# Kernel optimization log

Measured on AMD Instinct MI355X. Metric: run time of the kernel, lower is better.

## Reference

```python
import jax, jax.numpy as jnp
import numpy as np

N_NODES = 50000
NEG_SLOPE = 0.2


def _gat_conv(x, src, dst, W, a_src, a_dst, b, num_nodes):
    # W: [H*C, F_in]; a_src/a_dst: [H, C]; b: [H*C]
    H, C = a_src.shape
    xp = (x @ W.T).reshape(num_nodes, H, C)              # [N,H,C]
    alpha_s = jnp.sum(xp * a_src[None], axis=-1)          # [N,H]
    alpha_d = jnp.sum(xp * a_dst[None], axis=-1)          # [N,H]
    e = jax.nn.leaky_relu(alpha_s[src] + alpha_d[dst], NEG_SLOPE)  # [E,H]
    # segment softmax over incoming edges of each dst node (self-loops guarantee non-empty segments)
    m = jax.ops.segment_max(e, dst, num_segments=num_nodes)
    e = jnp.exp(e - m[dst])
    s = jax.ops.segment_sum(e, dst, num_segments=num_nodes)
    alpha = e / s[dst]                                    # [E,H]
    out = jax.ops.segment_sum(alpha[:, :, None] * xp[src], dst, num_segments=num_nodes)  # [N,H,C]
    return out.reshape(num_nodes, H * C) + b


def setup_inputs() -> dict:
    key = jax.random.key(0)
    ks = jax.random.split(key, 12)
    N, E, F_in, HID, H, Z = N_NODES, 800000, 128, 64, 2, 32
    sc = 0.1
    return {
        "features": jax.random.normal(ks[0], (N, F_in), jnp.float32),
        "edges": jax.random.randint(ks[1], (2, E), 0, N, jnp.int32),
        "W1": jax.random.normal(ks[2], (H * HID, F_in), jnp.float32) * sc,
        "a_src1": jax.random.normal(ks[3], (H, HID), jnp.float32) * sc,
        "a_dst1": jax.random.normal(ks[4], (H, HID), jnp.float32) * sc,
        "b1": jnp.zeros((H * HID,), jnp.float32),
        "W_mu": jax.random.normal(ks[5], (Z, H * HID), jnp.float32) * sc,
        "a_src_mu": jax.random.normal(ks[6], (1, Z), jnp.float32) * sc,
        "a_dst_mu": jax.random.normal(ks[7], (1, Z), jnp.float32) * sc,
        "b_mu": jnp.zeros((Z,), jnp.float32),
        "W_std": jax.random.normal(ks[8], (Z, H * HID), jnp.float32) * sc,
        "a_src_std": jax.random.normal(ks[9], (1, Z), jnp.float32) * sc,
        "a_dst_std": jax.random.normal(ks[10], (1, Z), jnp.float32) * sc,
        "b_std": jnp.zeros((Z,), jnp.float32),
    }


def reference(features, edges, W1, a_src1, a_dst1, b1, W_mu, a_src_mu, a_dst_mu, b_mu, W_std, a_src_std, a_dst_std, b_std):
    N = features.shape[0]
    loops = jnp.arange(N, dtype=edges.dtype)
    src = jnp.concatenate([edges[0], loops])  # add self loops (PyG default)
    dst = jnp.concatenate([edges[1], loops])
    h = _gat_conv(features, src, dst, W1, a_src1, a_dst1, b1, N)
    h = jax.nn.relu(h)  # dropout p=0.0 -> identity
    mu = _gat_conv(h, src, dst, W_mu, a_src_mu, a_dst_mu, b_mu, N)
    std = _gat_conv(h, src, dst, W_std, a_src_std, a_dst_std, b_std, N)
    return (mu, std)
```

## Files before the change

kernel.cpp:

```cpp
#include <hip/hip_runtime.h>
#include <math.h>

#define N_NODES 50000
#define N_EDGES 800000
#define ET (N_EDGES + N_NODES)
#define KD 128
#define Z 32
#define SH 7
#define BW 128
#define NBUCK ((N_NODES + BW - 1) / BW)
#define CHUNK 4096
#define NBLKA ((ET + CHUNK - 1) / CHUNK)
#define MTOT (NBUCK * NBLKA)
#define MBS ((MTOT + 1023) / 1024)

typedef __attribute__((ext_vector_type(8))) short bf16x8;
typedef __attribute__((ext_vector_type(4))) float f32x4;

static __device__ __forceinline__ float lrelu(float x){ return x > 0.f ? x : 0.2f*x; }
static __device__ __forceinline__ float lof(unsigned int u){ return __uint_as_float(u << 16); }
static __device__ __forceinline__ float hif(unsigned int u){ return __uint_as_float(u & 0xffff0000u); }
static __device__ __forceinline__ unsigned short f2bf(float f){
  unsigned int x = __float_as_uint(f);
  return (unsigned short)((x + 0x7fffu + ((x >> 16) & 1u)) >> 16);
}
static __device__ __forceinline__ unsigned int pack2(float lo, float hi){
  return (unsigned int)f2bf(lo) | ((unsigned int)f2bf(hi) << 16);
}

__global__ __launch_bounds__(256) void bhistA_kernel(const int* __restrict__ edges, int* __restrict__ M){
  int k = blockIdx.x, t = threadIdx.x;
  __shared__ int cnt[NBUCK];
  for(int b = t; b < NBUCK; b += 256) cnt[b] = 0;
  __syncthreads();
  int base = k*CHUNK;
  int lim = min(base + CHUNK, ET);
  for(int i = base + t; i < lim; i += 256){
    int d = (i < N_EDGES) ? edges[N_EDGES + i] : (i - N_EDGES);
    atomicAdd(&cnt[d >> SH], 1);
  }
  __syncthreads();
  for(int b = t; b < NBUCK; b += 256) M[b*NBLKA + k] = cnt[b];
}

__global__ __launch_bounds__(256) void scanM1_kernel(const int* __restrict__ M, int* __restrict__ bsumM){
  int b = blockIdx.x, t = threadIdx.x;
  int base = b*1024 + t*4;
  int s = 0;
  #pragma unroll
  for(int i=0;i<4;i++){ int n = base+i; if(n < MTOT) s += M[n]; }
  for(int off=32; off; off>>=1) s += __shfl_xor(s, off);
  __shared__ int ws[4];
  if((t&63)==0) ws[t>>6] = s;
  __syncthreads();
  if(t==0) bsumM[b] = ws[0]+ws[1]+ws[2]+ws[3];
}

__global__ __launch_bounds__(256) void scanM2_kernel(const int* __restrict__ bsumM, int* __restrict__ bpreM){
  __shared__ int sm[256];
  int t = threadIdx.x;
  int v = (t < MBS) ? bsumM[t] : 0;
  sm[t] = v;
  __syncthreads();
  for(int off=1; off<256; off<<=1){
    int u = (t >= off) ? sm[t-off] : 0;
    __syncthreads();
    sm[t] += u;
    __syncthreads();
  }
  if(t < MBS) bpreM[t] = sm[t] - v;
}

__global__ __launch_bounds__(256) void scanM3_kernel(const int* __restrict__ M, const int* __restrict__ bpreM,
                                                     int* __restrict__ Mpos){
  int b = blockIdx.x, t = threadIdx.x;
  int lane = t & 63, wv = t >> 6;
  int base = b*1024 + t*4;
  int d[4]; int s = 0;
  #pragma unroll
  for(int i=0;i<4;i++){ int n = base+i; d[i] = (n < MTOT) ? M[n] : 0; s += d[i]; }
  int v = s;
  for(int off=1; off<64; off<<=1){
    int u = __shfl_up(v, off);
    if(lane >= off) v += u;
  }
  int texcl = v - s;
  __shared__ int wtot[4];
  if(lane == 63) wtot[wv] = v;
  __syncthreads();
  int woff = 0;
  for(int i=0;i<wv;i++) woff += wtot[i];
  int run = bpreM[b] + woff + texcl;
  #pragma unroll
  for(int i=0;i<4;i++){
    int n = base+i;
    if(n < MTOT){ Mpos[n] = run; run += d[i]; }
  }
}

__global__ __launch_bounds__(256) void bplaceA_kernel(const int* __restrict__ edges, const int* __restrict__ Mpos,
                                                      int2* __restrict__ etmp){
  int k = blockIdx.x, t = threadIdx.x;
  __shared__ int cur[NBUCK];
  for(int b = t; b < NBUCK; b += 256) cur[b] = Mpos[b*NBLKA + k];
  __syncthreads();
  int base = k*CHUNK;
  int lim = min(base + CHUNK, ET);
  for(int i = base + t; i < lim; i += 256){
    int s, d;
    if(i < N_EDGES){ s = edges[i]; d = edges[N_EDGES+i]; } else { s = d = i - N_EDGES; }
    int pos = atomicAdd(&cur[d >> SH], 1);
    etmp[pos] = make_int2(s, d);
  }
}

__global__ __launch_bounds__(256) void bfin_kernel(const int* __restrict__ Mpos, const int2* __restrict__ etmp,
                                                   int* __restrict__ rowptr, int* __restrict__ esrc,
                                                   int* __restrict__ edst){
  int b = blockIdx.x, t = threadIdx.x;
  __shared__ int cnt[BW];
  __shared__ int pre[BW];
  __shared__ int lcur[BW];
  if(t < BW) cnt[t] = 0;
  if(b == 0 && t < 32) esrc[ET + t] = 0;
  __syncthreads();
  int beg = Mpos[b*NBLKA];
  int end = (b+1 < NBUCK) ? Mpos[(b+1)*NBLKA] : ET;
  for(int i = beg + t; i < end; i += 256) atomicAdd(&cnt[etmp[i].y & (BW-1)], 1);
  __syncthreads();
  if(t < BW) pre[t] = cnt[t];
  __syncthreads();
  for(int off=1; off<BW; off<<=1){
    int u = 0;
    if(t < BW && t >= off) u = pre[t-off];
    __syncthreads();
    if(t < BW) pre[t] += u;
    __syncthreads();
  }
  if(t < BW){
    int excl = pre[t] - cnt[t];
    int node = b*BW + t;
    if(node < N_NODES) rowptr[node] = beg + excl;
    lcur[t] = beg + excl;
  }
  if(b == 0 && t == 255) rowptr[N_NODES] = ET;
  __syncthreads();
  for(int i = beg + t; i < end; i += 256){
    int2 e = etmp[i];
    int pos = atomicAdd(&lcur[e.y & (BW-1)], 1);
    esrc[pos] = e.x;
    edst[pos] = e.y;
  }
}

__global__ __launch_bounds__(256) void wconv_kernel(const float* __restrict__ W1,
                                                    const float* __restrict__ Wmu, const float* __restrict__ Wst,
                                                    unsigned short* __restrict__ Wb1, unsigned short* __restrict__ Wb2){
  int i = blockIdx.x*256 + threadIdx.x;
  if(i < 128*KD) Wb1[i] = f2bf(W1[i]);
  if(i < 64*KD) Wb2[i] = f2bf(i < 32*KD ? Wmu[i] : Wst[i - 32*KD]);
}

__global__ __launch_bounds__(256) void mmt1_kernel(const float* __restrict__ X,
                                                   const unsigned short* __restrict__ Wb,
                                                   const float* __restrict__ asv, const float* __restrict__ adv,
                                                   unsigned short* __restrict__ outb,
                                                   float* __restrict__ as1, float* __restrict__ ad1){
  constexpr int OC = 128, CT = 8;
  int t = threadIdx.x;
  int w = t >> 6, L = t & 63;
  int col = L & 15, quad = L >> 4;
  int row0 = blockIdx.x*64 + w*16;
  int rA = row0 + col;
  if(rA >= N_NODES) rA = N_NODES-1;

  f32x4 acc[CT];
  #pragma unroll
  for(int ct=0;ct<CT;ct++) acc[ct] = (f32x4){0.f,0.f,0.f,0.f};

  #pragma unroll
  for(int kc=0;kc<4;kc++){
    int k0 = kc*32 + quad*8;
    const float* Xf = X + (size_t)rA*KD + k0;
    float4 p = *(const float4*)Xf;
    float4 q = *(const float4*)(Xf + 4);
    bf16x8 a;
    a[0] = (short)f2bf(p.x); a[1] = (short)f2bf(p.y);
    a[2] = (short)f2bf(p.z); a[3] = (short)f2bf(p.w);
    a[4] = (short)f2bf(q.x); a[5] = (short)f2bf(q.y);
    a[6] = (short)f2bf(q.z); a[7] = (short)f2bf(q.w);
    #pragma unroll
    for(int ct=0;ct<CT;ct++){
      bf16x8 b = *(const bf16x8*)(Wb + (size_t)(ct*16 + col)*KD + k0);
      acc[ct] = __builtin_amdgcn_mfma_f32_16x16x32_bf16(a, b, acc[ct], 0, 0, 0);
    }
  }

  float av[CT], dv[CT];
  #pragma unroll
  for(int ct=0;ct<CT;ct++){ av[ct] = asv[ct*16 + col]; dv[ct] = adv[ct*16 + col]; }

  #pragma unroll
  for(int r=0;r<4;r++){
    int row = row0 + quad*4 + r;
    #pragma unroll
    for(int ct=0;ct<CT;ct++)
      if(row < N_NODES) outb[(size_t)row*OC + ct*16 + col] = f2bf(acc[ct][r]);
    float s0 = acc[0][r]*av[0] + acc[1][r]*av[1] + acc[2][r]*av[2] + acc[3][r]*av[3];
    float s1 = acc[4][r]*av[4] + acc[5][r]*av[5] + acc[6][r]*av[6] + acc[7][r]*av[7];
    float d0 = acc[0][r]*dv[0] + acc[1][r]*dv[1] + acc[2][r]*dv[2] + acc[3][r]*dv[3];
    float d1 = acc[4][r]*dv[4] + acc[5][r]*dv[5] + acc[6][r]*dv[6] + acc[7][r]*dv[7];
    #pragma unroll
    for(int off=1; off<16; off<<=1){
      s0 += __shfl_xor(s0, off); s1 += __shfl_xor(s1, off);
      d0 += __shfl_xor(d0, off); d1 += __shfl_xor(d1, off);
    }
    if(col == 0 && row < N_NODES){
      as1[row*2] = s0; as1[row*2+1] = s1;
      ad1[row*2] = d0; ad1[row*2+1] = d1;
    }
  }
}

__global__ __launch_bounds__(256) void mmt2_kernel(const unsigned short* __restrict__ Xb,
                                                   const unsigned short* __restrict__ Wb,
                                                   const float* __restrict__ asmu, const float* __restrict__ admu,
                                                   const float* __restrict__ asst, const float* __restrict__ adst,
                                                   unsigned short* __restrict__ outb,
                                                   float* __restrict__ as2, float* __restrict__ ad2){
  constexpr int OC = 64, CT = 4;
  int t = threadIdx.x;
  int w = t >> 6, L = t & 63;
  int col = L & 15, quad = L >> 4;
  int row0 = blockIdx.x*64 + w*16;
  int rA = row0 + col;
  if(rA >= N_NODES) rA = N_NODES-1;

  f32x4 acc[CT];
  #pragma unroll
  for(int ct=0;ct<CT;ct++) acc[ct] = (f32x4){0.f,0.f,0.f,0.f};

  #pragma unroll
  for(int kc=0;kc<4;kc++){
    int k0 = kc*32 + quad*8;
    bf16x8 a = *(const bf16x8*)(Xb + (size_t)rA*KD + k0);
    #pragma unroll
    for(int ct=0;ct<CT;ct++){
      bf16x8 b = *(const bf16x8*)(Wb + (size_t)(ct*16 + col)*KD + k0);
      acc[ct] = __builtin_amdgcn_mfma_f32_16x16x32_bf16(a, b, acc[ct], 0, 0, 0);
    }
  }

  float av[CT], dv[CT];
  #pragma unroll
  for(int ct=0;ct<CT;ct++){
    av[ct] = (ct < 2) ? asmu[ct*16 + col] : asst[(ct-2)*16 + col];
    dv[ct] = (ct < 2) ? admu[ct*16 + col] : adst[(ct-2)*16 + col];
  }

  #pragma unroll
  for(int r=0;r<4;r++){
    int row = row0 + quad*4 + r;
    #pragma unroll
    for(int ct=0;ct<CT;ct++)
      if(row < N_NODES) outb[(size_t)row*OC + ct*16 + col] = f2bf(acc[ct][r]);
    float smu = acc[0][r]*av[0] + acc[1][r]*av[1];
    float sst = acc[2][r]*av[2] + acc[3][r]*av[3];
    float dmu = acc[0][r]*dv[0] + acc[1][r]*dv[1];
    float dst = acc[2][r]*dv[2] + acc[3][r]*dv[3];
    #pragma unroll
    for(int off=1; off<16; off<<=1){
      smu += __shfl_xor(smu, off); sst += __shfl_xor(sst, off);
      dmu += __shfl_xor(dmu, off); dst += __shfl_xor(dst, off);
    }
    if(col == 0 && row < N_NODES){
      as2[row*2] = smu; as2[row*2+1] = sst;
      ad2[row*2] = dmu; ad2[row*2+1] = dst;
    }
  }
}

__global__ __launch_bounds__(256) void wcalc_kernel(const int* __restrict__ esrc, const int* __restrict__ edst,
                                                    const float* __restrict__ as, const float* __restrict__ ad,
                                                    float2* __restrict__ wp){
  int i = blockIdx.x*256 + threadIdx.x;
  if(i >= ET) return;
  int s = esrc[i], d = edst[i];
  float2 a = ((const float2*)as)[s];
  float2 b = ((const float2*)ad)[d];
  wp[i] = make_float2(__expf(lrelu(a.x + b.x)), __expf(lrelu(a.y + b.y)));
}

__global__ __launch_bounds__(256) void agg1_kernel(const int* __restrict__ rowptr, const int* __restrict__ esrc,
                                                   const float2* __restrict__ wp,
                                                   const uint4* __restrict__ xb4,
                                                   const float* __restrict__ b1, uint4* __restrict__ hb4){
  int node = blockIdx.x*4 + (threadIdx.x>>6);
  int l = threadIdx.x & 63;
  if(node >= N_NODES) return;
  int g = l >> 4, c = l & 15;
  int beg = rowptr[node], end = rowptr[node+1];
  int n = end - beg;
  float a0=0.f,a1=0.f,a2=0.f,a3=0.f,a4=0.f,a5=0.f,a6=0.f,a7=0.f;
  float s0=0.f, s1=0.f;

#define S1_STEP(IDX) { \
    int e_ = esrc[(IDX)]; \
    float2 w_ = wp[(IDX)]; \
    uint4 u_ = xb4[(size_t)e_*16 + c]; \
    s0 += w_.x; s1 += w_.y; \
    float vv = (c < 8) ? w_.x : w_.y; \
    a0 += vv*lof(u_.x); a1 += vv*hif(u_.x); \
    a2 += vv*lof(u_.y); a3 += vv*hif(u_.y); \
    a4 += vv*lof(u_.z); a5 += vv*hif(u_.z); \
    a6 += vv*lof(u_.w); a7 += vv*hif(u_.w); }

#define S1_STEPM(IDX) { \
    int e_ = esrc[(IDX)]; \
    float2 w_ = wp[(IDX)]; \
    uint4 u_ = xb4[(size_t)e_*16 + c]; \
    float wx_ = ((IDX) < end) ? w_.x : 0.f; \
    float wy_ = ((IDX) < end) ? w_.y : 0.f; \
    s0 += wx_; s1 += wy_; \
    float vv = (c < 8) ? wx_ : wy_; \
    a0 += vv*lof(u_.x); a1 += vv*hif(u_.x); \
    a2 += vv*lof(u_.y); a3 += vv*hif(u_.y); \
    a4 += vv*lof(u_.z); a5 += vv*hif(u_.z); \
    a6 += vv*lof(u_.w); a7 += vv*hif(u_.w); }

  int i = beg;
  int nfull = n & ~7;
  for(; i < beg + nfull; i += 8){
    S1_STEP(i + g)
    S1_STEP(i + 4 + g)
  }
  if(i < end){
    S1_STEPM(i + g)
    S1_STEPM(i + 4 + g)
  }
#undef S1_STEP
#undef S1_STEPM

  #pragma unroll
  for(int off=16; off<64; off<<=1){
    s0 += __shfl_xor(s0,off); s1 += __shfl_xor(s1,off);
    a0 += __shfl_xor(a0,off); a1 += __shfl_xor(a1,off);
    a2 += __shfl_xor(a2,off); a3 += __shfl_xor(a3,off);
    a4 += __shfl_xor(a4,off); a5 += __shfl_xor(a5,off);
    a6 += __shfl_xor(a6,off); a7 += __shfl_xor(a7,off);
  }
  if(g == 0){
    float sd = (c < 8) ? s0 : s1;
    float inv = 1.f / sd;
    const float4* bp = (const float4*)(b1 + 8*c);
    float4 bl = bp[0], bh = bp[1];
    float r0 = fmaxf(a0*inv + bl.x, 0.f);
    float r1 = fmaxf(a1*inv + bl.y, 0.f);
    float r2 = fmaxf(a2*inv + bl.z, 0.f);
    float r3 = fmaxf(a3*inv + bl.w, 0.f);
    float r4 = fmaxf(a4*inv + bh.x, 0.f);
    float r5 = fmaxf(a5*inv + bh.y, 0.f);
    float r6 = fmaxf(a6*inv + bh.z, 0.f);
    float r7 = fmaxf(a7*inv + bh.w, 0.f);
    uint4 o;
    o.x = pack2(r0, r1); o.y = pack2(r2, r3);
    o.z = pack2(r4, r5); o.w = pack2(r6, r7);
    hb4[(size_t)node*16 + c] = o;
  }
}

__global__ __launch_bounds__(256) void agg2_kernel(const int* __restrict__ rowptr, const int* __restrict__ esrc,
                                                   const float2* __restrict__ wp,
                                                   const uint4* __restrict__ xb4,
                                                   const float* __restrict__ bmu, const float* __restrict__ bst,
                                                   float* __restrict__ out){
  int node = blockIdx.x*4 + (threadIdx.x>>6);
  int l = threadIdx.x & 63;
  if(node >= N_NODES) return;
  int g = l >> 3, c = l & 7;
  int beg = rowptr[node], end = rowptr[node+1];
  int n = end - beg;
  float a0=0.f,a1=0.f,a2=0.f,a3=0.f,a4=0.f,a5=0.f,a6=0.f,a7=0.f;
  float smu=0.f, sst=0.f;

#define S2_STEP(IDX) { \
    int e_ = esrc[(IDX)]; \
    float2 w_ = wp[(IDX)]; \
    uint4 u_ = xb4[(size_t)e_*8 + c]; \
    smu += w_.x; sst += w_.y; \
    float vv = (c < 4) ? w_.x : w_.y; \
    a0 += vv*lof(u_.x); a1 += vv*hif(u_.x); \
    a2 += vv*lof(u_.y); a3 += vv*hif(u_.y); \
    a4 += vv*lof(u_.z); a5 += vv*hif(u_.z); \
    a6 += vv*lof(u_.w); a7 += vv*hif(u_.w); }

#define S2_STEPM(IDX) { \
    int e_ = esrc[(IDX)]; \
    float2 w_ = wp[(IDX)]; \
    uint4 u_ = xb4[(size_t)e_*8 + c]; \
    float wx_ = ((IDX) < end) ? w_.x : 0.f; \
    float wy_ = ((IDX) < end) ? w_.y : 0.f; \
    smu += wx_; sst += wy_; \
    float vv = (c < 4) ? wx_ : wy_; \
    a0 += vv*lof(u_.x); a1 += vv*hif(u_.x); \
    a2 += vv*lof(u_.y); a3 += vv*hif(u_.y); \
    a4 += vv*lof(u_.z); a5 += vv*hif(u_.z); \
    a6 += vv*lof(u_.w); a7 += vv*hif(u_.w); }

  int i = beg;
  int nfull = n & ~15;
  for(; i < beg + nfull; i += 16){
    S2_STEP(i + g)
    S2_STEP(i + 8 + g)
  }
  if(i < end){
    S2_STEPM(i + g)
    S2_STEPM(i + 8 + g)
  }
#undef S2_STEP
#undef S2_STEPM

  #pragma unroll
  for(int off=8; off<64; off<<=1){
    smu += __shfl_xor(smu,off); sst += __shfl_xor(sst,off);
    a0 += __shfl_xor(a0,off); a1 += __shfl_xor(a1,off);
    a2 += __shfl_xor(a2,off); a3 += __shfl_xor(a3,off);
    a4 += __shfl_xor(a4,off); a5 += __shfl_xor(a5,off);
    a6 += __shfl_xor(a6,off); a7 += __shfl_xor(a7,off);
  }
  if(g == 0){
    float sd = (c < 4) ? smu : sst;
    float inv = 1.f / sd;
    const float* bb = (c < 4) ? (bmu + 8*c) : (bst + 8*(c-4));
    float4 bl = *(const float4*)bb;
    float4 bh = *(const float4*)(bb + 4);
    float* op = (c < 4) ? (out + (size_t)node*Z + 8*c)
                        : (out + (size_t)N_NODES*Z + (size_t)node*Z + 8*(c-4));
    float4 r0, r1;
    r0.x = a0*inv + bl.x; r0.y = a1*inv + bl.y;
    r0.z = a2*inv + bl.z; r0.w = a3*inv + bl.w;
    r1.x = a4*inv + bh.x; r1.y = a5*inv + bh.y;
    r1.z = a6*inv + bh.z; r1.w = a7*inv + bh.w;
    *(float4*)op = r0;
    *((float4*)op + 1) = r1;
  }
}

extern "C" void kernel_launch(void* const* d_in, const int* in_sizes, int n_in,
                              void* d_out, int out_size, void* d_ws, size_t ws_size,
                              hipStream_t stream){
  const float* x    = (const float*)d_in[0];
  const int*   edges= (const int*)d_in[1];
  const float* W1   = (const float*)d_in[2];
  const float* as1v = (const float*)d_in[3];
  const float* ad1v = (const float*)d_in[4];
  const float* b1   = (const float*)d_in[5];
  const float* Wmu  = (const float*)d_in[6];
  const float* asmu = (const float*)d_in[7];
  const float* admu = (const float*)d_in[8];
  const float* bmu  = (const float*)d_in[9];
  const float* Wst  = (const float*)d_in[10];
  const float* asst = (const float*)d_in[11];
  const float* adst = (const float*)d_in[12];
  const float* bst  = (const float*)d_in[13];
  float* out = (float*)d_out;

  char* p = (char*)d_ws;
  auto alloc = [&](size_t bytes)->char*{ char* r = p; p += (bytes + 255) & ~size_t(255); return r; };
  int*   M      = (int*)  alloc((size_t)MTOT*4);
  int*   Mpos   = (int*)  alloc((size_t)MTOT*4);
  int*   bsumM  = (int*)  alloc((size_t)MBS*4);
  int*   bpreM  = (int*)  alloc((size_t)MBS*4);
  int2*  etmp   = (int2*) alloc((size_t)(ET+32)*8);
  int*   esrc   = (int*)  alloc((size_t)(ET+32)*4);
  int*   edst   = (int*)  alloc((size_t)ET*4);
  int*   rowptr = (int*)  alloc((size_t)(N_NODES+1)*4);
  unsigned short* Wb1 = (unsigned short*)alloc((size_t)128*KD*2);
  unsigned short* Wb2 = (unsigned short*)alloc((size_t)64*KD*2);
  unsigned short* xpb1 = (unsigned short*)alloc((size_t)N_NODES*128*2);
  float* as1    = (float*)alloc((size_t)N_NODES*2*4);
  float* ad1    = (float*)alloc((size_t)N_NODES*2*4);
  unsigned short* hb = (unsigned short*)alloc((size_t)N_NODES*128*2);
  float* as2    = (float*)alloc((size_t)N_NODES*2*4);
  float* ad2    = (float*)alloc((size_t)N_NODES*2*4);
  unsigned short* xpb2 = xpb1;
  float2* wedge = (float2*)etmp;

  bhistA_kernel  <<<NBLKA, 256, 0, stream>>>(edges, M);
  scanM1_kernel  <<<MBS, 256, 0, stream>>>(M, bsumM);
  scanM2_kernel  <<<1, 256, 0, stream>>>(bsumM, bpreM);
  scanM3_kernel  <<<MBS, 256, 0, stream>>>(M, bpreM, Mpos);
  bplaceA_kernel <<<NBLKA, 256, 0, stream>>>(edges, Mpos, etmp);
  bfin_kernel    <<<NBUCK, 256, 0, stream>>>(Mpos, etmp, rowptr, esrc, edst);

  wconv_kernel   <<<(128*KD + 255)/256, 256, 0, stream>>>(W1, Wmu, Wst, Wb1, Wb2);

  mmt1_kernel  <<<(N_NODES+63)/64, 256, 0, stream>>>(x, Wb1, as1v, ad1v, xpb1, as1, ad1);
  wcalc_kernel <<<(ET+255)/256, 256, 0, stream>>>(esrc, edst, as1, ad1, wedge);
  agg1_kernel  <<<(N_NODES+3)/4, 256, 0, stream>>>(rowptr, esrc, wedge, (const uint4*)xpb1, b1, (uint4*)hb);

  mmt2_kernel  <<<(N_NODES+63)/64, 256, 0, stream>>>(hb, Wb2, asmu, admu, asst, adst, xpb1, as2, ad2);
  wcalc_kernel <<<(ET+255)/256, 256, 0, stream>>>(esrc, edst, as2, ad2, wedge);
  agg2_kernel  <<<(N_NODES+3)/4, 256, 0, stream>>>(rowptr, esrc, wedge, (const uint4*)xpb2, bmu, bst, out);
}
```

Measured before the change: 238.8 us.

## Replace two-level bucket sort CSR build with global atomic histogram and scatter

The CSR construction changes from a six-kernel two-level bucketed counting sort to a simpler pipeline: a global per-node atomic degree histogram, a single-block 1024-thread scan, and a scatter that uses global atomics on per-node cursors. Degree zeroing and padding init are folded into the weight-conversion kernel, so there are fewer launches and no intermediate etmp pass. In exchange it relies on global atomics with possible contention, a serial single-block scan, and nondeterministic edge order within each row, which can change floating-point summation order. The edge-weight buffer gets its own allocation instead of aliasing etmp.

```diff
diff --git a/kernel.cpp b/kernel.cpp
--- a/kernel.cpp
+++ b/kernel.cpp
@@ -6,13 +6,6 @@
 #define ET (N_EDGES + N_NODES)
 #define KD 128
 #define Z 32
-#define SH 7
-#define BW 128
-#define NBUCK ((N_NODES + BW - 1) / BW)
-#define CHUNK 4096
-#define NBLKA ((ET + CHUNK - 1) / CHUNK)
-#define MTOT (NBUCK * NBLKA)
-#define MBS ((MTOT + 1023) / 1024)
 
 typedef __attribute__((ext_vector_type(8))) short bf16x8;
 typedef __attribute__((ext_vector_type(4))) float f32x4;
@@ -28,137 +21,67 @@
   return (unsigned int)f2bf(lo) | ((unsigned int)f2bf(hi) << 16);
 }
 
-__global__ __launch_bounds__(256) void bhistA_kernel(const int* __restrict__ edges, int* __restrict__ M){
-  int k = blockIdx.x, t = threadIdx.x;
-  __shared__ int cnt[NBUCK];
-  for(int b = t; b < NBUCK; b += 256) cnt[b] = 0;
-  __syncthreads();
-  int base = k*CHUNK;
-  int lim = min(base + CHUNK, ET);
-  for(int i = base + t; i < lim; i += 256){
-    int d = (i < N_EDGES) ? edges[N_EDGES + i] : (i - N_EDGES);
-    atomicAdd(&cnt[d >> SH], 1);
-  }
-  __syncthreads();
-  for(int b = t; b < NBUCK; b += 256) M[b*NBLKA + k] = cnt[b];
-}
-
-__global__ __launch_bounds__(256) void scanM1_kernel(const int* __restrict__ M, int* __restrict__ bsumM){
-  int b = blockIdx.x, t = threadIdx.x;
-  int base = b*1024 + t*4;
+__global__ __launch_bounds__(256) void wconv_kernel(const float* __restrict__ W1,
+                                                    const float* __restrict__ Wmu, const float* __restrict__ Wst,
+                                                    unsigned short* __restrict__ Wb1, unsigned short* __restrict__ Wb2,
+                                                    int* __restrict__ deg, int* __restrict__ esrc){
+  int i = blockIdx.x*256 + threadIdx.x;
+  if(i < 128*KD) Wb1[i] = f2bf(W1[i]);
+  if(i < 64*KD) Wb2[i] = f2bf(i < 32*KD ? Wmu[i] : Wst[i - 32*KD]);
+  if(i < N_NODES) deg[i] = 0;
+  if(i < 32) esrc[ET + i] = 0;
+}
+
+__global__ __launch_bounds__(256) void ghist_kernel(const int* __restrict__ edges, int* __restrict__ deg){
+  int i = blockIdx.x*256 + threadIdx.x;
+  if(i >= ET) return;
+  int d = (i < N_EDGES) ? edges[N_EDGES + i] : (i - N_EDGES);
+  atomicAdd(&deg[d], 1);
+}
+
+__global__ __launch_bounds__(1024) void gscan_kernel(const int* __restrict__ deg,
+                                                     int* __restrict__ rowptr, int* __restrict__ cur){
+  constexpr int CHK = (N_NODES + 1023) / 1024;
+  int t = threadIdx.x;
+  int lane = t & 63, wv = t >> 6;
+  int base = t * CHK;
+  int d[CHK];
   int s = 0;
   #pragma unroll
-  for(int i=0;i<4;i++){ int n = base+i; if(n < MTOT) s += M[n]; }
-  for(int off=32; off; off>>=1) s += __shfl_xor(s, off);
-  __shared__ int ws[4];
-  if((t&63)==0) ws[t>>6] = s;
-  __syncthreads();
-  if(t==0) bsumM[b] = ws[0]+ws[1]+ws[2]+ws[3];
-}
-
-__global__ __launch_bounds__(256) void scanM2_kernel(const int* __restrict__ bsumM, int* __restrict__ bpreM){
-  __shared__ int sm[256];
-  int t = threadIdx.x;
-  int v = (t < MBS) ? bsumM[t] : 0;
-  sm[t] = v;
-  __syncthreads();
-  for(int off=1; off<256; off<<=1){
-    int u = (t >= off) ? sm[t-off] : 0;
-    __syncthreads();
-    sm[t] += u;
-    __syncthreads();
-  }
-  if(t < MBS) bpreM[t] = sm[t] - v;
-}
-
-__global__ __launch_bounds__(256) void scanM3_kernel(const int* __restrict__ M, const int* __restrict__ bpreM,
-                                                     int* __restrict__ Mpos){
-  int b = blockIdx.x, t = threadIdx.x;
-  int lane = t & 63, wv = t >> 6;
-  int base = b*1024 + t*4;
-  int d[4]; int s = 0;
-  #pragma unroll
-  for(int i=0;i<4;i++){ int n = base+i; d[i] = (n < MTOT) ? M[n] : 0; s += d[i]; }
+  for(int i=0;i<CHK;i++){
+    int n = base + i;
+    int v = (n < N_NODES) ? deg[n] : 0;
+    d[i] = v; s += v;
+  }
   int v = s;
   for(int off=1; off<64; off<<=1){
     int u = __shfl_up(v, off);
     if(lane >= off) v += u;
   }
-  int texcl = v - s;
-  __shared__ int wtot[4];
-  if(lane == 63) wtot[wv] = v;
+  __shared__ int wt[16];
+  if(lane == 63) wt[wv] = v;
   __syncthreads();
   int woff = 0;
-  for(int i=0;i<wv;i++) woff += wtot[i];
-  int run = bpreM[b] + woff + texcl;
-  #pragma unroll
-  for(int i=0;i<4;i++){
-    int n = base+i;
-    if(n < MTOT){ Mpos[n] = run; run += d[i]; }
-  }
-}
-
-__global__ __launch_bounds__(256) void bplaceA_kernel(const int* __restrict__ edges, const int* __restrict__ Mpos,
-                                                      int2* __restrict__ etmp){
-  int k = blockIdx.x, t = threadIdx.x;
-  __shared__ int cur[NBUCK];
-  for(int b = t; b < NBUCK; b += 256) cur[b] = Mpos[b*NBLKA + k];
-  __syncthreads();
-  int base = k*CHUNK;
-  int lim = min(base + CHUNK, ET);
-  for(int i = base + t; i < lim; i += 256){
-    int s, d;
-    if(i < N_EDGES){ s = edges[i]; d = edges[N_EDGES+i]; } else { s = d = i - N_EDGES; }
-    int pos = atomicAdd(&cur[d >> SH], 1);
-    etmp[pos] = make_int2(s, d);
-  }
-}
-
-__global__ __launch_bounds__(256) void bfin_kernel(const int* __restrict__ Mpos, const int2* __restrict__ etmp,
-                                                   int* __restrict__ rowptr, int* __restrict__ esrc,
-                                                   int* __restrict__ edst){
-  int b = blockIdx.x, t = threadIdx.x;
-  __shared__ int cnt[BW];
-  __shared__ int pre[BW];
-  __shared__ int lcur[BW];
-  if(t < BW) cnt[t] = 0;
-  if(b == 0 && t < 32) esrc[ET + t] = 0;
-  __syncthreads();
-  int beg = Mpos[b*NBLKA];
-  int end = (b+1 < NBUCK) ? Mpos[(b+1)*NBLKA] : ET;
-  for(int i = beg + t; i < end; i += 256) atomicAdd(&cnt[etmp[i].y & (BW-1)], 1);
-  __syncthreads();
-  if(t < BW) pre[t] = cnt[t];
-  __syncthreads();
-  for(int off=1; off<BW; off<<=1){
-    int u = 0;
-    if(t < BW && t >= off) u = pre[t-off];
-    __syncthreads();
-    if(t < BW) pre[t] += u;
-    __syncthreads();
-  }
-  if(t < BW){
-    int excl = pre[t] - cnt[t];
-    int node = b*BW + t;
-    if(node < N_NODES) rowptr[node] = beg + excl;
-    lcur[t] = beg + excl;
-  }
-  if(b == 0 && t == 255) rowptr[N_NODES] = ET;
-  __syncthreads();
-  for(int i = beg + t; i < end; i += 256){
-    int2 e = etmp[i];
-    int pos = atomicAdd(&lcur[e.y & (BW-1)], 1);
-    esrc[pos] = e.x;
-    edst[pos] = e.y;
-  }
-}
-
-__global__ __launch_bounds__(256) void wconv_kernel(const float* __restrict__ W1,
-                                                    const float* __restrict__ Wmu, const float* __restrict__ Wst,
-                                                    unsigned short* __restrict__ Wb1, unsigned short* __restrict__ Wb2){
+  for(int i=0;i<wv;i++) woff += wt[i];
+  int run = woff + (v - s);
+  #pragma unroll
+  for(int i=0;i<CHK;i++){
+    int n = base + i;
+    if(n < N_NODES){ rowptr[n] = run; cur[n] = run; }
+    run += d[i];
+  }
+  if(t == 1023) rowptr[N_NODES] = run;
+}
+
+__global__ __launch_bounds__(256) void gplace_kernel(const int* __restrict__ edges, int* __restrict__ cur,
+                                                     int* __restrict__ esrc, int* __restrict__ edst){
   int i = blockIdx.x*256 + threadIdx.x;
-  if(i < 128*KD) Wb1[i] = f2bf(W1[i]);
-  if(i < 64*KD) Wb2[i] = f2bf(i < 32*KD ? Wmu[i] : Wst[i - 32*KD]);
+  if(i >= ET) return;
+  int s, d;
+  if(i < N_EDGES){ s = edges[i]; d = edges[N_EDGES+i]; } else { s = d = i - N_EDGES; }
+  int pos = atomicAdd(&cur[d], 1);
+  esrc[pos] = s;
+  edst[pos] = d;
 }
 
 __global__ __launch_bounds__(256) void mmt1_kernel(const float* __restrict__ X,
@@ -467,14 +390,12 @@
 
   char* p = (char*)d_ws;
   auto alloc = [&](size_t bytes)->char*{ char* r = p; p += (bytes + 255) & ~size_t(255); return r; };
-  int*   M      = (int*)  alloc((size_t)MTOT*4);
-  int*   Mpos   = (int*)  alloc((size_t)MTOT*4);
-  int*   bsumM  = (int*)  alloc((size_t)MBS*4);
-  int*   bpreM  = (int*)  alloc((size_t)MBS*4);
-  int2*  etmp   = (int2*) alloc((size_t)(ET+32)*8);
+  int*   deg    = (int*)  alloc((size_t)N_NODES*4);
+  int*   cur    = (int*)  alloc((size_t)N_NODES*4);
+  int*   rowptr = (int*)  alloc((size_t)(N_NODES+1)*4);
   int*   esrc   = (int*)  alloc((size_t)(ET+32)*4);
   int*   edst   = (int*)  alloc((size_t)ET*4);
-  int*   rowptr = (int*)  alloc((size_t)(N_NODES+1)*4);
+  float2* wedge = (float2*)alloc((size_t)(ET+32)*8);
   unsigned short* Wb1 = (unsigned short*)alloc((size_t)128*KD*2);
   unsigned short* Wb2 = (unsigned short*)alloc((size_t)64*KD*2);
   unsigned short* xpb1 = (unsigned short*)alloc((size_t)N_NODES*128*2);
@@ -484,16 +405,11 @@
   float* as2    = (float*)alloc((size_t)N_NODES*2*4);
   float* ad2    = (float*)alloc((size_t)N_NODES*2*4);
   unsigned short* xpb2 = xpb1;
-  float2* wedge = (float2*)etmp;
-
-  bhistA_kernel  <<<NBLKA, 256, 0, stream>>>(edges, M);
-  scanM1_kernel  <<<MBS, 256, 0, stream>>>(M, bsumM);
-  scanM2_kernel  <<<1, 256, 0, stream>>>(bsumM, bpreM);
-  scanM3_kernel  <<<MBS, 256, 0, stream>>>(M, bpreM, Mpos);
-  bplaceA_kernel <<<NBLKA, 256, 0, stream>>>(edges, Mpos, etmp);
-  bfin_kernel    <<<NBUCK, 256, 0, stream>>>(Mpos, etmp, rowptr, esrc, edst);
-
-  wconv_kernel   <<<(128*KD + 255)/256, 256, 0, stream>>>(W1, Wmu, Wst, Wb1, Wb2);
+
+  wconv_kernel  <<<(N_NODES+255)/256, 256, 0, stream>>>(W1, Wmu, Wst, Wb1, Wb2, deg, esrc);
+  ghist_kernel  <<<(ET+255)/256, 256, 0, stream>>>(edges, deg);
+  gscan_kernel  <<<1, 1024, 0, stream>>>(deg, rowptr, cur);
+  gplace_kernel <<<(ET+255)/256, 256, 0, stream>>>(edges, cur, esrc, edst);
 
   mmt1_kernel  <<<(N_NODES+63)/64, 256, 0, stream>>>(x, Wb1, as1v, ad1v, xpb1, as1, ad1);
   wcalc_kernel <<<(ET+255)/256, 256, 0, stream>>>(esrc, edst, as1, ad1, wedge);
```

Measured after the change: 363.8 us. +52.3%, slower.

## Merge independent CSR-build and GEMM kernels into shared launches, pack edge temp

Applied to the files above, without the earlier changes.

Launches the bucket histogram together with the weight bf16 conversion in one grid, and the bucket placement together with the first-layer GEMM in another, with the block index picking the role. This removes two launches and lets independent work overlap. The temporary edge array shrinks from int2 to a packed 32-bit word (17-bit source, local destination in the high bits), which halves its traffic in placement and finalisation. The edge-weight buffer now gets its own allocation because it can no longer alias the smaller temp array. Packing assumes node ids fit in 17 bits.

```diff
diff --git a/kernel.cpp b/kernel.cpp
--- a/kernel.cpp
+++ b/kernel.cpp
@@ -13,6 +13,7 @@
 #define NBLKA ((ET + CHUNK - 1) / CHUNK)
 #define MTOT (NBUCK * NBLKA)
 #define MBS ((MTOT + 1023) / 1024)
+#define WCB 64
 
 typedef __attribute__((ext_vector_type(8))) short bf16x8;
 typedef __attribute__((ext_vector_type(4))) float f32x4;
@@ -28,8 +29,8 @@
   return (unsigned int)f2bf(lo) | ((unsigned int)f2bf(hi) << 16);
 }
 
-__global__ __launch_bounds__(256) void bhistA_kernel(const int* __restrict__ edges, int* __restrict__ M){
-  int k = blockIdx.x, t = threadIdx.x;
+static __device__ __forceinline__ void bhistA_body(int k, const int* __restrict__ edges, int* __restrict__ M){
+  int t = threadIdx.x;
   __shared__ int cnt[NBUCK];
   for(int b = t; b < NBUCK; b += 256) cnt[b] = 0;
   __syncthreads();
@@ -41,6 +42,22 @@
   }
   __syncthreads();
   for(int b = t; b < NBUCK; b += 256) M[b*NBLKA + k] = cnt[b];
+}
+
+static __device__ __forceinline__ void wconv_body(int bid, const float* __restrict__ W1,
+                                                  const float* __restrict__ Wmu, const float* __restrict__ Wst,
+                                                  unsigned short* __restrict__ Wb1, unsigned short* __restrict__ Wb2){
+  int i = bid*256 + threadIdx.x;
+  if(i < 128*KD) Wb1[i] = f2bf(W1[i]);
+  if(i < 64*KD) Wb2[i] = f2bf(i < 32*KD ? Wmu[i] : Wst[i - 32*KD]);
+}
+
+__global__ __launch_bounds__(256) void packA_kernel(const int* __restrict__ edges, int* __restrict__ M,
+                                                    const float* __restrict__ W1,
+                                                    const float* __restrict__ Wmu, const float* __restrict__ Wst,
+                                                    unsigned short* __restrict__ Wb1, unsigned short* __restrict__ Wb2){
+  if(blockIdx.x < NBLKA) bhistA_body(blockIdx.x, edges, M);
+  else                   wconv_body(blockIdx.x - NBLKA, W1, Wmu, Wst, Wb1, Wb2);
 }
 
 __global__ __launch_bounds__(256) void scanM1_kernel(const int* __restrict__ M, int* __restrict__ bsumM){
@@ -98,9 +115,9 @@
   }
 }
 
-__global__ __launch_bounds__(256) void bplaceA_kernel(const int* __restrict__ edges, const int* __restrict__ Mpos,
-                                                      int2* __restrict__ etmp){
-  int k = blockIdx.x, t = threadIdx.x;
+static __device__ __forceinline__ void bplaceA_body(int k, const int* __restrict__ edges,
+                                                    const int* __restrict__ Mpos, unsigned int* __restrict__ etmp){
+  int t = threadIdx.x;
   __shared__ int cur[NBUCK];
   for(int b = t; b < NBUCK; b += 256) cur[b] = Mpos[b*NBLKA + k];
   __syncthreads();
@@ -110,67 +127,20 @@
     int s, d;
     if(i < N_EDGES){ s = edges[i]; d = edges[N_EDGES+i]; } else { s = d = i - N_EDGES; }
     int pos = atomicAdd(&cur[d >> SH], 1);
-    etmp[pos] = make_int2(s, d);
-  }
-}
-
-__global__ __launch_bounds__(256) void bfin_kernel(const int* __restrict__ Mpos, const int2* __restrict__ etmp,
-                                                   int* __restrict__ rowptr, int* __restrict__ esrc,
-                                                   int* __restrict__ edst){
-  int b = blockIdx.x, t = threadIdx.x;
-  __shared__ int cnt[BW];
-  __shared__ int pre[BW];
-  __shared__ int lcur[BW];
-  if(t < BW) cnt[t] = 0;
-  if(b == 0 && t < 32) esrc[ET + t] = 0;
-  __syncthreads();
-  int beg = Mpos[b*NBLKA];
-  int end = (b+1 < NBUCK) ? Mpos[(b+1)*NBLKA] : ET;
-  for(int i = beg + t; i < end; i += 256) atomicAdd(&cnt[etmp[i].y & (BW-1)], 1);
-  __syncthreads();
-  if(t < BW) pre[t] = cnt[t];
-  __syncthreads();
-  for(int off=1; off<BW; off<<=1){
-    int u = 0;
-    if(t < BW && t >= off) u = pre[t-off];
-    __syncthreads();
-    if(t < BW) pre[t] += u;
-    __syncthreads();
-  }
-  if(t < BW){
-    int excl = pre[t] - cnt[t];
-    int node = b*BW + t;
-    if(node < N_NODES) rowptr[node] = beg + excl;
-    lcur[t] = beg + excl;
-  }
-  if(b == 0 && t == 255) rowptr[N_NODES] = ET;
-  __syncthreads();
-  for(int i = beg + t; i < end; i += 256){
-    int2 e = etmp[i];
-    int pos = atomicAdd(&lcur[e.y & (BW-1)], 1);
-    esrc[pos] = e.x;
-    edst[pos] = e.y;
-  }
-}
-
-__global__ __launch_bounds__(256) void wconv_kernel(const float* __restrict__ W1,
-                                                    const float* __restrict__ Wmu, const float* __restrict__ Wst,
-                                                    unsigned short* __restrict__ Wb1, unsigned short* __restrict__ Wb2){
-  int i = blockIdx.x*256 + threadIdx.x;
-  if(i < 128*KD) Wb1[i] = f2bf(W1[i]);
-  if(i < 64*KD) Wb2[i] = f2bf(i < 32*KD ? Wmu[i] : Wst[i - 32*KD]);
-}
-
-__global__ __launch_bounds__(256) void mmt1_kernel(const float* __restrict__ X,
-                                                   const unsigned short* __restrict__ Wb,
-                                                   const float* __restrict__ asv, const float* __restrict__ adv,
-                                                   unsigned short* __restrict__ outb,
-                                                   float* __restrict__ as1, float* __restrict__ ad1){
+    etmp[pos] = (unsigned int)s | ((unsigned int)(d & (BW-1)) << 17);
+  }
+}
+
+static __device__ __forceinline__ void mmt1_body(int bid, const float* __restrict__ X,
+                                                 const unsigned short* __restrict__ Wb,
+                                                 const float* __restrict__ asv, const float* __restrict__ adv,
+                                                 unsigned short* __restrict__ outb,
+                                                 float* __restrict__ as1, float* __restrict__ ad1){
   constexpr int OC = 128, CT = 8;
   int t = threadIdx.x;
   int w = t >> 6, L = t & 63;
   int col = L & 15, quad = L >> 4;
-  int row0 = blockIdx.x*64 + w*16;
+  int row0 = bid*64 + w*16;
   int rA = row0 + col;
   if(rA >= N_NODES) rA = N_NODES-1;
 
@@ -222,6 +192,56 @@
   }
 }
 
+__global__ __launch_bounds__(256) void packB_kernel(const int* __restrict__ edges, const int* __restrict__ Mpos,
+                                                    unsigned int* __restrict__ etmp,
+                                                    const float* __restrict__ X, const unsigned short* __restrict__ Wb,
+                                                    const float* __restrict__ asv, const float* __restrict__ adv,
+                                                    unsigned short* __restrict__ outb,
+                                                    float* __restrict__ as1, float* __restrict__ ad1){
+  if(blockIdx.x < NBLKA) bplaceA_body(blockIdx.x, edges, Mpos, etmp);
+  else                   mmt1_body(blockIdx.x - NBLKA, X, Wb, asv, adv, outb, as1, ad1);
+}
+
+__global__ __launch_bounds__(256) void bfin_kernel(const int* __restrict__ Mpos, const unsigned int* __restrict__ etmp,
+                                                   int* __restrict__ rowptr, int* __restrict__ esrc,
+                                                   int* __restrict__ edst){
+  int b = blockIdx.x, t = threadIdx.x;
+  __shared__ int cnt[BW];
+  __shared__ int pre[BW];
+  __shared__ int lcur[BW];
+  if(t < BW) cnt[t] = 0;
+  if(b == 0 && t < 32) esrc[ET + t] = 0;
+  __syncthreads();
+  int beg = Mpos[b*NBLKA];
+  int end = (b+1 < NBUCK) ? Mpos[(b+1)*NBLKA] : ET;
+  for(int i = beg + t; i < end; i += 256) atomicAdd(&cnt[etmp[i] >> 17], 1);
+  __syncthreads();
+  if(t < BW) pre[t] = cnt[t];
+  __syncthreads();
+  for(int off=1; off<BW; off<<=1){
+    int u = 0;
+    if(t < BW && t >= off) u = pre[t-off];
+    __syncthreads();
+    if(t < BW) pre[t] += u;
+    __syncthreads();
+  }
+  if(t < BW){
+    int excl = pre[t] - cnt[t];
+    int node = b*BW + t;
+    if(node < N_NODES) rowptr[node] = beg + excl;
+    lcur[t] = beg + excl;
+  }
+  if(b == 0 && t == 255) rowptr[N_NODES] = ET;
+  __syncthreads();
+  for(int i = beg + t; i < end; i += 256){
+    unsigned int e = etmp[i];
+    int lo = (int)(e >> 17);
+    int pos = atomicAdd(&lcur[lo], 1);
+    esrc[pos] = (int)(e & 0x1FFFFu);
+    edst[pos] = b*BW + lo;
+  }
+}
+
 __global__ __launch_bounds__(256) void mmt2_kernel(const unsigned short* __restrict__ Xb,
                                                    const unsigned short* __restrict__ Wb,
                                                    const float* __restrict__ asmu, const float* __restrict__ admu,
@@ -471,10 +491,11 @@
   int*   Mpos   = (int*)  alloc((size_t)MTOT*4);
   int*   bsumM  = (int*)  alloc((size_t)MBS*4);
   int*   bpreM  = (int*)  alloc((size_t)MBS*4);
-  int2*  etmp   = (int2*) alloc((size_t)(ET+32)*8);
+  unsigned int* etmp = (unsigned int*)alloc((size_t)ET*4);
   int*   esrc   = (int*)  alloc((size_t)(ET+32)*4);
   int*   edst   = (int*)  alloc((size_t)ET*4);
   int*   rowptr = (int*)  alloc((size_t)(N_NODES+1)*4);
+  float2* wedge = (float2*)alloc((size_t)(ET+32)*8);
   unsigned short* Wb1 = (unsigned short*)alloc((size_t)128*KD*2);
   unsigned short* Wb2 = (unsigned short*)alloc((size_t)64*KD*2);
   unsigned short* xpb1 = (unsigned short*)alloc((size_t)N_NODES*128*2);
@@ -484,18 +505,15 @@
   float* as2    = (float*)alloc((size_t)N_NODES*2*4);
   float* ad2    = (float*)alloc((size_t)N_NODES*2*4);
   unsigned short* xpb2 = xpb1;
-  float2* wedge = (float2*)etmp;
-
-  bhistA_kernel  <<<NBLKA, 256, 0, stream>>>(edges, M);
-  scanM1_kernel  <<<MBS, 256, 0, stream>>>(M, bsumM);
-  scanM2_kernel  <<<1, 256, 0, stream>>>(bsumM, bpreM);
-  scanM3_kernel  <<<MBS, 256, 0, stream>>>(M, bpreM, Mpos);
-  bplaceA_kernel <<<NBLKA, 256, 0, stream>>>(edges, Mpos, etmp);
-  bfin_kernel    <<<NBUCK, 256, 0, stream>>>(Mpos, etmp, rowptr, esrc, edst);
-
-  wconv_kernel   <<<(128*KD + 255)/256, 256, 0, stream>>>(W1, Wmu, Wst, Wb1, Wb2);
-
-  mmt1_kernel  <<<(N_NODES+63)/64, 256, 0, stream>>>(x, Wb1, as1v, ad1v, xpb1, as1, ad1);
+
+  packA_kernel  <<<NBLKA + WCB, 256, 0, stream>>>(edges, M, W1, Wmu, Wst, Wb1, Wb2);
+  scanM1_kernel <<<MBS, 256, 0, stream>>>(M, bsumM);
+  scanM2_kernel <<<1, 256, 0, stream>>>(bsumM, bpreM);
+  scanM3_kernel <<<MBS, 256, 0, stream>>>(M, bpreM, Mpos);
+  packB_kernel  <<<NBLKA + (N_NODES+63)/64, 256, 0, stream>>>(edges, Mpos, etmp,
+                                                              x, Wb1, as1v, ad1v, xpb1, as1, ad1);
+  bfin_kernel   <<<NBUCK, 256, 0, stream>>>(Mpos, etmp, rowptr, esrc, edst);
+
   wcalc_kernel <<<(ET+255)/256, 256, 0, stream>>>(esrc, edst, as1, ad1, wedge);
   agg1_kernel  <<<(N_NODES+3)/4, 256, 0, stream>>>(rowptr, esrc, wedge, (const uint4*)xpb1, b1, (uint4*)hb);
 
```

Result: faster. 227.0 us (-5.0%).
